# Optimization experiments

Measured on AMD Instinct MI355X. Metric: run time of the kernel, lower is better.

Reference implementation:

```python
import jax, jax.numpy as jnp
import numpy as np

B, N, C = 8, 4096, 768
H = 4 * C  # mlp hidden
EPS = 1e-7
LN_EPS = 1e-5


def _ln(x, g, b):
    mu = jnp.mean(x, axis=-1, keepdims=True)
    var = jnp.mean((x - mu) ** 2, axis=-1, keepdims=True)
    return (x - mu) * jax.lax.rsqrt(var + LN_EPS) * g + b


def _mlp(z, w1, b1, w2, b2):
    return jax.nn.gelu(z @ w1 + b1, approximate=False) @ w2 + b2


def setup_inputs() -> dict:
    key = jax.random.key(0)
    ks = jax.random.split(key, 16)
    s = 1.0 / np.sqrt(C)
    inp = {
        "x": jax.random.normal(ks[0], (B, N, C), jnp.float32),
        "y": jax.random.normal(ks[1], (B, N, C), jnp.float32),
        "mask": jax.random.randint(ks[2], (B, N, 1), 0, 2).astype(jnp.float32),
        "h": 64,
        "w": 64,
        "ln1_g": jnp.ones((C,), jnp.float32),
        "ln1_b": jnp.zeros((C,), jnp.float32),
        "Wq": jax.random.normal(ks[3], (C, C), jnp.float32) * s,
        "Wk": jax.random.normal(ks[4], (C, C), jnp.float32) * s,
        "Wv": jax.random.normal(ks[5], (C, C), jnp.float32) * s,
        "Wpx": jax.random.normal(ks[6], (2 * C, C), jnp.float32) * s,
        "Wpy": jax.random.normal(ks[7], (2 * C, C), jnp.float32) * s,
        "ln2_g": jnp.ones((C,), jnp.float32),
        "ln2_b": jnp.zeros((C,), jnp.float32),
        "fx1_w": jax.random.normal(ks[8], (C, H), jnp.float32) * s,
        "fx1_b": jnp.zeros((H,), jnp.float32),
        "fx2_w": jax.random.normal(ks[9], (H, C), jnp.float32) / np.sqrt(H),
        "fx2_b": jnp.zeros((C,), jnp.float32),
        "fy1_w": jax.random.normal(ks[10], (C, H), jnp.float32) * s,
        "fy1_b": jnp.zeros((H,), jnp.float32),
        "fy2_w": jax.random.normal(ks[11], (H, C), jnp.float32) / np.sqrt(H),
        "fy2_b": jnp.zeros((C,), jnp.float32),
    }
    return inp


def _minmax(s):
    mn = jnp.min(s, axis=1, keepdims=True)
    mx = jnp.max(s, axis=1, keepdims=True)
    return (s - mn) / (mx - mn + EPS)


def reference(x, y, mask, h, w, ln1_g, ln1_b, Wq, Wk, Wv, Wpx, Wpy,
              ln2_g, ln2_b, fx1_w, fx1_b, fx2_w, fx2_b, fy1_w, fy1_b, fy2_w, fy2_b):
    b, n, c = x.shape
    m = mask.reshape(b, n, 1)  # binary mask per token
    xn = _ln(x, ln1_g, ln1_b)
    yn = _ln(y, ln1_g, ln1_b)
    q = yn @ Wq  # (b,n,c)
    k = xn @ Wk
    v = xn @ Wv
    # masked GAP pools (Weighted_GAP): (b,c)
    fg = jnp.sum(q * m, axis=1) / (jnp.sum(m, axis=1) + 5e-4)
    bg = jnp.sum(q * (1.0 - m), axis=1) / (jnp.sum(1.0 - m, axis=1) + 5e-4)
    k_nrm = jnp.linalg.norm(k, axis=2)  # (b,n)
    fg_nrm = jnp.linalg.norm(fg, axis=1, keepdims=True)  # (b,1)
    bg_nrm = jnp.linalg.norm(bg, axis=1, keepdims=True)
    fg_s = jnp.einsum('bnc,bc->bn', k, fg) / (k_nrm * fg_nrm + EPS)
    bg_s = jnp.einsum('bnc,bc->bn', k, bg) / (k_nrm * bg_nrm + EPS)
    scores = _minmax(fg_s) - _minmax(bg_s)  # (b,n)
    pseudo_mask = scores.reshape(b, 1, h, w)
    attn = jax.nn.softmax(jnp.where(scores < 0, scores - 100.0, scores), axis=1)
    query_pro = jnp.einsum('bn,bnc->bc', attn, v)  # (b,c)
    qp_nrm = jnp.linalg.norm(query_pro, axis=1, keepdims=True)
    sim = jnp.sum(query_pro * fg, axis=1, keepdims=True) / (qp_nrm * fg_nrm + EPS)
    sim = (sim + 1.0) * 0.5  # (b,1)
    pro = sim * fg + (1.0 - sim) * query_pro  # (b,c)
    pro_b = jnp.broadcast_to(pro[:, None, :], x.shape)
    xo = x + jnp.concatenate([x, pro_b], axis=-1) @ Wpx
    yo = y + jnp.concatenate([y, pro_b], axis=-1) @ Wpy
    xo = xo + _mlp(_ln(xo, ln2_g, ln2_b), fx1_w, fx1_b, fx2_w, fx2_b)
    yo = yo + _mlp(_ln(yo, ln2_g, ln2_b), fy1_w, fy1_b, fy2_w, fy2_b)
    return (xo, yo, pseudo_mask)
```

## Files before the change

kernel.cpp:

```cpp
#include <hip/hip_runtime.h>
#include <math.h>

#define B_ 8
#define N_ 4096
#define C_ 768
#define H_ 3072
#define M_ (B_*N_)
#define NSPLIT 16

typedef unsigned short u16;
typedef unsigned int u32;
typedef __attribute__((ext_vector_type(8))) __bf16 bf16x8;
typedef __attribute__((ext_vector_type(4))) float f32x4;
typedef __attribute__((ext_vector_type(4))) unsigned short u16x4;
typedef __attribute__((ext_vector_type(8))) unsigned short u16x8;

__device__ __forceinline__ u16 f2bf(float f){
  u32 u = __float_as_uint(f);
  u32 r = (u + 0x7FFFu + ((u >> 16) & 1u)) >> 16;
  return (u16)r;
}
__device__ __forceinline__ float bf2f(u16 h){
  return __uint_as_float(((u32)h) << 16);
}
__device__ __forceinline__ void gload_lds16(const void* g, void* l){
  __builtin_amdgcn_global_load_lds((const __attribute__((address_space(1))) void*)g,
                                   (__attribute__((address_space(3))) void*)l, 16, 0, 0);
}

template<int EPI>
__global__ __launch_bounds__(512, 4) void gemm_bf16(
    const u16* __restrict__ A, const u16* __restrict__ BT,
    int K, int N, int NBN,
    void* __restrict__ outp,
    const float* __restrict__ resid,
    const float* __restrict__ rowv,
    const float* __restrict__ bias)
{
  __shared__ u16 lds[2][12288];
  const int tid = threadIdx.x;
  const int wid = tid >> 6, lane = tid & 63;

  const int nwg = gridDim.x;
  int wg = blockIdx.x;
  wg = (wg & 7) * (nwg >> 3) + (wg >> 3);
  const int GMN = 8 * NBN;
  const int g = wg / GMN, r = wg % GMN;
  const int bm = (g*8 + (r & 7)) * 256;
  const int bn = (r >> 3) * 128;

  const int wr = wid >> 1, wc = wid & 1;

  f32x4 acc[4][4];
#pragma unroll
  for (int i=0;i<4;i++)
#pragma unroll
    for (int j=0;j<4;j++) acc[i][j] = (f32x4){0.f,0.f,0.f,0.f};

  const u16* agp0 = A  + (size_t)(bm + (tid>>2))*K + (tid&3)*8;
  const u16* agp1 = A  + (size_t)(bm + 128 + (tid>>2))*K + (tid&3)*8;
  const u16* bgp0 = BT + (size_t)(bn + (tid>>2))*K + (tid&3)*8;

  auto STAGE = [&](int c){
    char* base = (char*)lds[c] + wid*1024;
    gload_lds16(agp0, base);
    gload_lds16(agp1, base + 8192);
    gload_lds16(bgp0, base + 16384);
    agp0 += 32; agp1 += 32; bgp0 += 32;
  };

  const int aoff = (wr*64 + (lane&15))*32 + ((lane>>4)<<3);
  const int boff = 8192 + (wc*64 + (lane&15))*32 + ((lane>>4)<<3);

  const int nk = K >> 5;
  STAGE(0);
  __syncthreads();
  int cur = 0;
  for (int kk=0; kk<nk; kk++){
    if (kk+1 < nk) STAGE(cur^1);
    bf16x8 av[4], bv[4];
    const u16* pa = &lds[cur][aoff];
    const u16* pb = &lds[cur][boff];
#pragma unroll
    for (int i=0;i<4;i++){
      av[i] = *reinterpret_cast<const bf16x8*>(pa + i*512);
      bv[i] = *reinterpret_cast<const bf16x8*>(pb + i*512);
    }
#pragma unroll
    for (int i=0;i<4;i++)
#pragma unroll
      for (int j=0;j<4;j++)
        acc[i][j] = __builtin_amdgcn_mfma_f32_16x16x32_bf16(av[i], bv[j], acc[i][j], 0, 0, 0);
    __syncthreads();
    cur ^= 1;
  }

  const int col0 = bn + wc*64 + (lane & 15);
  const int row0 = bm + wr*64 + ((lane >> 4) << 2);
#pragma unroll
  for (int i=0;i<4;i++){
#pragma unroll
    for (int j=0;j<4;j++){
#pragma unroll
      for (int r2=0;r2<4;r2++){
        const int row = row0 + i*16 + r2;
        const int cj  = col0 + j*16;
        const size_t o = (size_t)row*N + cj;
        const float va = acc[i][j][r2];
        if constexpr (EPI == 0){
          ((u16*)outp)[o] = f2bf(va);
        } else if constexpr (EPI == 1){
          ((float*)outp)[o] = resid[o] + va + rowv[(row >> 12)*N + cj];
        } else if constexpr (EPI == 2){
          const float z = va + bias[cj];
          ((u16*)outp)[o] = f2bf(0.5f*z*(1.0f + erff(z*0.70710678f)));
        } else {
          float* po = (float*)outp + o;
          *po += va + bias[cj];
        }
      }
    }
  }
}

__device__ __forceinline__ void ln_row(const float* __restrict__ p,
    const float* __restrict__ gam, const float* __restrict__ bet,
    u16* __restrict__ op, int lane)
{
  float4 v0 = *reinterpret_cast<const float4*>(p + lane*4);
  float4 v1 = *reinterpret_cast<const float4*>(p + lane*4 + 256);
  float4 v2 = *reinterpret_cast<const float4*>(p + lane*4 + 512);
  float s  = v0.x+v0.y+v0.z+v0.w + v1.x+v1.y+v1.z+v1.w + v2.x+v2.y+v2.z+v2.w;
  float sq = v0.x*v0.x+v0.y*v0.y+v0.z*v0.z+v0.w*v0.w
           + v1.x*v1.x+v1.y*v1.y+v1.z*v1.z+v1.w*v1.w
           + v2.x*v2.x+v2.y*v2.y+v2.z*v2.z+v2.w*v2.w;
#pragma unroll
  for (int o=32;o>0;o>>=1){ s += __shfl_xor(s,o); sq += __shfl_xor(sq,o); }
  const float mu = s * (1.f/C_);
  const float rs = rsqrtf(sq*(1.f/C_) - mu*mu + 1e-5f);
  float4 g0 = *reinterpret_cast<const float4*>(gam + lane*4);
  float4 g1 = *reinterpret_cast<const float4*>(gam + lane*4 + 256);
  float4 g2 = *reinterpret_cast<const float4*>(gam + lane*4 + 512);
  float4 b0 = *reinterpret_cast<const float4*>(bet + lane*4);
  float4 b1 = *reinterpret_cast<const float4*>(bet + lane*4 + 256);
  float4 b2 = *reinterpret_cast<const float4*>(bet + lane*4 + 512);
  u16x4 o0, o1, o2;
  o0[0]=f2bf((v0.x-mu)*rs*g0.x+b0.x); o0[1]=f2bf((v0.y-mu)*rs*g0.y+b0.y);
  o0[2]=f2bf((v0.z-mu)*rs*g0.z+b0.z); o0[3]=f2bf((v0.w-mu)*rs*g0.w+b0.w);
  o1[0]=f2bf((v1.x-mu)*rs*g1.x+b1.x); o1[1]=f2bf((v1.y-mu)*rs*g1.y+b1.y);
  o1[2]=f2bf((v1.z-mu)*rs*g1.z+b1.z); o1[3]=f2bf((v1.w-mu)*rs*g1.w+b1.w);
  o2[0]=f2bf((v2.x-mu)*rs*g2.x+b2.x); o2[1]=f2bf((v2.y-mu)*rs*g2.y+b2.y);
  o2[2]=f2bf((v2.z-mu)*rs*g2.z+b2.z); o2[3]=f2bf((v2.w-mu)*rs*g2.w+b2.w);
  *reinterpret_cast<u16x4*>(op + lane*4)       = o0;
  *reinterpret_cast<u16x4*>(op + lane*4 + 256) = o1;
  *reinterpret_cast<u16x4*>(op + lane*4 + 512) = o2;
}

__global__ __launch_bounds__(256) void ln_fwd(const float* __restrict__ in,
    const float* __restrict__ gam, const float* __restrict__ bet,
    u16* __restrict__ out)
{
  const int row  = blockIdx.x*4 + (threadIdx.x >> 6);
  const int lane = threadIdx.x & 63;
  ln_row(in + (size_t)row*C_, gam, bet, out + (size_t)row*C_, lane);
}

__global__ __launch_bounds__(256) void ln_fwd2(const float* __restrict__ inx,
    const float* __restrict__ iny, const float* __restrict__ gam,
    const float* __restrict__ bet, u16* __restrict__ outx, u16* __restrict__ outy)
{
  const int row  = blockIdx.x*4 + (threadIdx.x >> 6);
  const int lane = threadIdx.x & 63;
  const float* in = blockIdx.y ? iny : inx;
  u16* out = blockIdx.y ? outy : outx;
  ln_row(in + (size_t)row*C_, gam, bet, out + (size_t)row*C_, lane);
}

__global__ __launch_bounds__(256) void cvt2_bf16(const float* __restrict__ inx,
    const float* __restrict__ iny, u16* __restrict__ outx, u16* __restrict__ outy,
    int n4)
{
  int i = blockIdx.x*256 + threadIdx.x;
  const float* in = blockIdx.y ? iny : inx;
  u16* out = blockIdx.y ? outy : outx;
  if (i < n4){
    float4 v = reinterpret_cast<const float4*>(in)[i];
    u16x4 o; o[0]=f2bf(v.x); o[1]=f2bf(v.y); o[2]=f2bf(v.z); o[3]=f2bf(v.w);
    *reinterpret_cast<u16x4*>(out + (size_t)i*4) = o;
  }
}

__device__ __forceinline__ void tr_tile(const float* __restrict__ in,
    u16* __restrict__ outp, int R, int Cc, int t)
{
  __shared__ float tile[32][33];
  const int tilesx = Cc >> 5;
  const int c0 = (t % tilesx)*32, r0 = (t / tilesx)*32;
  const int tx = threadIdx.x & 31, ty = threadIdx.x >> 5;
#pragma unroll
  for (int i=0;i<32;i+=8)
    tile[ty+i][tx] = in[(size_t)(r0+ty+i)*Cc + c0+tx];
  __syncthreads();
#pragma unroll
  for (int i=0;i<32;i+=8)
    outp[(size_t)(c0+ty+i)*R + r0+tx] = f2bf(tile[tx][ty+i]);
}

__global__ __launch_bounds__(256) void transpose_all(
    const float* Wk, const float* Wpx, const float* Wpy,
    const float* f1x, const float* f2x, const float* f1y, const float* f2y,
    u16* WkT, u16* WpxT, u16* WpyT, u16* f1xT, u16* f2xT, u16* f1yT, u16* f2yT)
{
  int t = blockIdx.x;
  if (t < 1728){
    const int m = t / 576; t -= m*576;
    const float* in = (m==0)?Wk:((m==1)?Wpx:Wpy);
    u16* o = (m==0)?WkT:((m==1)?WpxT:WpyT);
    tr_tile(in, o, C_, C_, t);
  } else {
    t -= 1728;
    const int m = t / 2304; t -= m*2304;
    if (m==0)      tr_tile(f1x, f1xT, C_, H_, t);
    else if (m==1) tr_tile(f2x, f2xT, H_, C_, t);
    else if (m==2) tr_tile(f1y, f1yT, C_, H_, t);
    else           tr_tile(f2y, f2yT, H_, C_, t);
  }
}

__global__ __launch_bounds__(256) void pool_partial(const u16* __restrict__ q,
    const float* __restrict__ mask, float* __restrict__ pm, float* __restrict__ pa,
    float* __restrict__ mpart)
{
  const int c = blockIdx.x*256 + threadIdx.x;
  const int b = blockIdx.y, z = blockIdx.z;
  const int n0 = z*(N_/NSPLIT);
  const u16* qp = q + ((size_t)b*N_ + n0)*C_ + c;
  const float* mp = mask + (size_t)b*N_ + n0;
  float am=0.f, aa=0.f, ms=0.f;
  for (int n=0;n<N_/NSPLIT;n++){
    float v = bf2f(qp[(size_t)n*C_]);
    float m = mp[n];
    am += v*m; aa += v; ms += m;
  }
  const size_t o = ((size_t)z*B_ + b)*C_ + c;
  pm[o]=am; pa[o]=aa;
  if (blockIdx.x==0 && threadIdx.x==0) mpart[z*B_+b] = ms;
}

__global__ __launch_bounds__(256) void proto_fused(const float* __restrict__ pm,
    const float* __restrict__ pa, const float* __restrict__ mpart,
    const float* __restrict__ Wq,
    float* __restrict__ fg, float* __restrict__ bg,
    float* __restrict__ fgn, float* __restrict__ bgn)
{
  __shared__ float fin[C_], bin[C_];
  __shared__ float red[8];
  const int b = blockIdx.x, tid = threadIdx.x;
  float msum_b = 0.f;
#pragma unroll
  for (int z=0;z<NSPLIT;z++) msum_b += mpart[z*B_+b];
  for (int c=tid;c<C_;c+=256){
    float sm=0.f, sa=0.f;
#pragma unroll
    for (int z=0;z<NSPLIT;z++){ size_t o=((size_t)z*B_+b)*C_+c; sm+=pm[o]; sa+=pa[o]; }
    fin[c] = sm/(msum_b + 5e-4f);
    bin[c] = (sa - sm)/((float)N_ - msum_b + 5e-4f);
  }
  __syncthreads();
  const int j0 = tid, j1 = tid+256, j2 = tid+512;
  float f0=0,f1=0,f2=0,g0=0,g1=0,g2=0;
  for (int c=0;c<C_;c++){
    const float* w = Wq + (size_t)c*C_;
    float fc = fin[c], bc = bin[c];
    float w0=w[j0], w1=w[j1], w2=w[j2];
    f0 += fc*w0; f1 += fc*w1; f2 += fc*w2;
    g0 += bc*w0; g1 += bc*w1; g2 += bc*w2;
  }
  fg[b*C_+j0]=f0; fg[b*C_+j1]=f1; fg[b*C_+j2]=f2;
  bg[b*C_+j0]=g0; bg[b*C_+j1]=g1; bg[b*C_+j2]=g2;
  float sf = f0*f0+f1*f1+f2*f2, sb = g0*g0+g1*g1+g2*g2;
#pragma unroll
  for (int o=32;o>0;o>>=1){ sf+=__shfl_down(sf,o); sb+=__shfl_down(sb,o); }
  if ((tid&63)==0){ red[tid>>6]=sf; red[4+(tid>>6)]=sb; }
  __syncthreads();
  if (tid==0){
    fgn[b]=sqrtf(red[0]+red[1]+red[2]+red[3]);
    bgn[b]=sqrtf(red[4]+red[5]+red[6]+red[7]);
  }
}

__global__ __launch_bounds__(256) void score_kernel(const u16* __restrict__ k,
    const float* __restrict__ fg, const float* __restrict__ bg,
    const float* __restrict__ fgn, const float* __restrict__ bgn,
    float* __restrict__ fg_s, float* __restrict__ bg_s)
{
  const int t = blockIdx.x*4 + (threadIdx.x >> 6);
  const int lane = threadIdx.x & 63;
  const int b = t >> 12;
  const u16* kp = k + (size_t)t*C_;
  u16x8 k8 = *reinterpret_cast<const u16x8*>(kp + lane*8);
  u16x4 k4 = *reinterpret_cast<const u16x4*>(kp + 512 + lane*4);
  const float* fgp = fg + b*C_;
  const float* bgp = bg + b*C_;
  float4 fa = *reinterpret_cast<const float4*>(fgp + lane*8);
  float4 fb = *reinterpret_cast<const float4*>(fgp + lane*8 + 4);
  float4 fc = *reinterpret_cast<const float4*>(fgp + 512 + lane*4);
  float4 ba = *reinterpret_cast<const float4*>(bgp + lane*8);
  float4 bb = *reinterpret_cast<const float4*>(bgp + lane*8 + 4);
  float4 bc = *reinterpret_cast<const float4*>(bgp + 512 + lane*4);
  float kv[12];
#pragma unroll
  for (int i=0;i<8;i++) kv[i] = bf2f(k8[i]);
#pragma unroll
  for (int i=0;i<4;i++) kv[8+i] = bf2f(k4[i]);
  float df = kv[0]*fa.x+kv[1]*fa.y+kv[2]*fa.z+kv[3]*fa.w
           + kv[4]*fb.x+kv[5]*fb.y+kv[6]*fb.z+kv[7]*fb.w
           + kv[8]*fc.x+kv[9]*fc.y+kv[10]*fc.z+kv[11]*fc.w;
  float db = kv[0]*ba.x+kv[1]*ba.y+kv[2]*ba.z+kv[3]*ba.w
           + kv[4]*bb.x+kv[5]*bb.y+kv[6]*bb.z+kv[7]*bb.w
           + kv[8]*bc.x+kv[9]*bc.y+kv[10]*bc.z+kv[11]*bc.w;
  float kk=0.f;
#pragma unroll
  for (int i=0;i<12;i++) kk += kv[i]*kv[i];
#pragma unroll
  for (int o=32;o>0;o>>=1){
    df+=__shfl_xor(df,o); db+=__shfl_xor(db,o); kk+=__shfl_xor(kk,o);
  }
  if (lane==0){
    const float kn = sqrtf(kk);
    fg_s[t] = df/(kn*fgn[b]+1e-7f);
    bg_s[t] = db/(kn*bgn[b]+1e-7f);
  }
}

__global__ __launch_bounds__(256) void minmax_kernel(const float* __restrict__ fg_s,
    const float* __restrict__ bg_s, float* __restrict__ mm)
{
  __shared__ float sm[16];
  const int b = blockIdx.x;
  float mnf=1e30f, mxf=-1e30f, mnb=1e30f, mxb=-1e30f;
  for (int i=threadIdx.x;i<N_;i+=256){
    float a = fg_s[(size_t)b*N_+i]; mnf=fminf(mnf,a); mxf=fmaxf(mxf,a);
    float c = bg_s[(size_t)b*N_+i]; mnb=fminf(mnb,c); mxb=fmaxf(mxb,c);
  }
#pragma unroll
  for (int o=32;o>0;o>>=1){
    mnf=fminf(mnf,__shfl_down(mnf,o)); mxf=fmaxf(mxf,__shfl_down(mxf,o));
    mnb=fminf(mnb,__shfl_down(mnb,o)); mxb=fmaxf(mxb,__shfl_down(mxb,o));
  }
  const int wid = threadIdx.x>>6;
  if ((threadIdx.x&63)==0){ sm[wid]=mnf; sm[4+wid]=mxf; sm[8+wid]=mnb; sm[12+wid]=mxb; }
  __syncthreads();
  if (threadIdx.x==0){
    mm[b*4+0]=fminf(fminf(sm[0],sm[1]),fminf(sm[2],sm[3]));
    mm[b*4+1]=fmaxf(fmaxf(sm[4],sm[5]),fmaxf(sm[6],sm[7]));
    mm[b*4+2]=fminf(fminf(sm[8],sm[9]),fminf(sm[10],sm[11]));
    mm[b*4+3]=fmaxf(fmaxf(sm[12],sm[13]),fmaxf(sm[14],sm[15]));
  }
}

__global__ __launch_bounds__(1024) void scorefin_fused(const float* __restrict__ fg_s,
    const float* __restrict__ bg_s, const float* __restrict__ mm,
    float* __restrict__ pseudo, float* __restrict__ escr, float* __restrict__ denom)
{
  __shared__ float sm[16];
  const int b = blockIdx.x, tid = threadIdx.x;
  const float mnf=mm[b*4+0], mxf=mm[b*4+1], mnb=mm[b*4+2], mxb=mm[b*4+3];
  const float rf = 1.f/(mxf-mnf+1e-7f), rb = 1.f/(mxb-mnb+1e-7f);
  float ps = 0.f;
#pragma unroll
  for (int i=0;i<4;i++){
    const int t = tid + i*1024;
    const size_t o = (size_t)b*N_ + t;
    const float s = (fg_s[o]-mnf)*rf - (bg_s[o]-mnb)*rb;
    pseudo[o] = s;
    const float e = expf(s < 0.f ? s - 100.f : s);
    escr[o] = e;
    ps += e;
  }
#pragma unroll
  for (int o=32;o>0;o>>=1) ps += __shfl_down(ps,o);
  if ((tid&63)==0) sm[tid>>6]=ps;
  __syncthreads();
  if (tid==0){
    float s=0.f;
#pragma unroll
    for (int w=0;w<16;w++) s+=sm[w];
    denom[b]=s;
  }
}

__global__ __launch_bounds__(256) void vpool_partial(const u16* __restrict__ xn,
    const float* __restrict__ e, float* __restrict__ pv)
{
  const int c = blockIdx.x*256 + threadIdx.x;
  const int b = blockIdx.y, z = blockIdx.z;
  const int n0 = z*(N_/NSPLIT);
  const u16* vp = xn + ((size_t)b*N_ + n0)*C_ + c;
  const float* ep = e + (size_t)b*N_ + n0;
  float acc=0.f;
  for (int n=0;n<N_/NSPLIT;n++) acc += bf2f(vp[(size_t)n*C_])*ep[n];
  pv[((size_t)z*B_+b)*C_+c] = acc;
}

__global__ __launch_bounds__(256) void pro_fused(const float* __restrict__ pv,
    const float* __restrict__ denom,
    const float* __restrict__ Wv, const float* __restrict__ Wpx,
    const float* __restrict__ Wpy,
    const float* __restrict__ fg, const float* __restrict__ fgn,
    float* __restrict__ rowx, float* __restrict__ rowy)
{
  __shared__ float vin[C_];
  __shared__ float red[8];
  __shared__ float simsh;
  const int b = blockIdx.x, tid = threadIdx.x;
  const float den = 1.f/denom[b];
  for (int c=tid;c<C_;c+=256){
    float s=0.f;
#pragma unroll
    for (int z=0;z<NSPLIT;z++) s += pv[((size_t)z*B_+b)*C_+c];
    vin[c] = s*den;
  }
  __syncthreads();
  const int j0 = tid, j1 = tid+256, j2 = tid+512;
  float q0=0,q1=0,q2=0;
  for (int c=0;c<C_;c++){
    const float* w = Wv + (size_t)c*C_;
    float vv = vin[c];
    q0 += vv*w[j0]; q1 += vv*w[j1]; q2 += vv*w[j2];
  }
  const float fg0 = fg[b*C_+j0], fg1 = fg[b*C_+j1], fg2 = fg[b*C_+j2];
  float d = q0*fg0 + q1*fg1 + q2*fg2;
  float qq = q0*q0 + q1*q1 + q2*q2;
#pragma unroll
  for (int o=32;o>0;o>>=1){ d+=__shfl_down(d,o); qq+=__shfl_down(qq,o); }
  if ((tid&63)==0){ red[tid>>6]=d; red[4+(tid>>6)]=qq; }
  __syncthreads();
  if (tid==0){
    float dd=red[0]+red[1]+red[2]+red[3], qs=red[4]+red[5]+red[6]+red[7];
    simsh = (dd/(sqrtf(qs)*fgn[b]+1e-7f)+1.f)*0.5f;
  }
  __syncthreads();
  const float sim = simsh;
  vin[j0] = sim*fg0 + (1.f-sim)*q0;
  vin[j1] = sim*fg1 + (1.f-sim)*q1;
  vin[j2] = sim*fg2 + (1.f-sim)*q2;
  __syncthreads();
  float rx0=0,rx1=0,rx2=0, ry0=0,ry1=0,ry2=0;
  for (int c=0;c<C_;c++){
    const float* wx = Wpx + (size_t)(C_+c)*C_;
    const float* wy = Wpy + (size_t)(C_+c)*C_;
    float pc = vin[c];
    rx0 += pc*wx[j0]; rx1 += pc*wx[j1]; rx2 += pc*wx[j2];
    ry0 += pc*wy[j0]; ry1 += pc*wy[j1]; ry2 += pc*wy[j2];
  }
  rowx[b*C_+j0]=rx0; rowx[b*C_+j1]=rx1; rowx[b*C_+j2]=rx2;
  rowy[b*C_+j0]=ry0; rowy[b*C_+j1]=ry1; rowy[b*C_+j2]=ry2;
}

extern "C" void kernel_launch(void* const* d_in, const int* in_sizes, int n_in,
                              void* d_out, int out_size, void* d_ws, size_t ws_size,
                              hipStream_t stream)
{
  const float* x     = (const float*)d_in[0];
  const float* y     = (const float*)d_in[1];
  const float* mask  = (const float*)d_in[2];
  const float* ln1_g = (const float*)d_in[5];
  const float* ln1_b = (const float*)d_in[6];
  const float* Wq    = (const float*)d_in[7];
  const float* Wk    = (const float*)d_in[8];
  const float* Wv    = (const float*)d_in[9];
  const float* Wpx   = (const float*)d_in[10];
  const float* Wpy   = (const float*)d_in[11];
  const float* ln2_g = (const float*)d_in[12];
  const float* ln2_b = (const float*)d_in[13];
  const float* fx1_w = (const float*)d_in[14];
  const float* fx1_b = (const float*)d_in[15];
  const float* fx2_w = (const float*)d_in[16];
  const float* fx2_b = (const float*)d_in[17];
  const float* fy1_w = (const float*)d_in[18];
  const float* fy1_b = (const float*)d_in[19];
  const float* fy2_w = (const float*)d_in[20];
  const float* fy2_b = (const float*)d_in[21];

  float* out    = (float*)d_out;
  float* out_xo = out;
  float* out_yo = out + (size_t)M_*C_;
  float* out_ps = out + 2*(size_t)M_*C_;

  char* ws = (char*)d_ws;
  const size_t ACT = (size_t)M_*C_;
  u16* R0  = (u16*)ws;
  u16* xnb = R0;
  u16* ynb = R0 + ACT;
  u16* kb  = R0 + 2*ACT;
  u16* hid = R0;
  u16* qb  = (u16*)(ws + 4*ACT*2);
  u16* wp  = (u16*)(ws + 5*ACT*2);
  u16* WkT  = wp;
  u16* WpxT = wp + 1*589824;
  u16* WpyT = wp + 2*589824;
  u16* fx1T = wp + 3*589824;
  u16* fx2T = fx1T + 2359296;
  u16* fy1T = fx2T + 2359296;
  u16* fy2T = fy1T + 2359296;
  float* st   = (float*)(ws + 5*ACT*2 + (size_t)(3*589824 + 4*2359296)*2);
  float* fgn  = st + 8;
  float* bgn  = st + 16;
  float* denom= st + 24;
  float* mm   = st + 32;
  float* fg   = st + 64;
  float* bg   = st + 6208;
  float* rowx = st + 24640;
  float* rowy = st + 30784;
  float* fg_s = st + 37056;
  float* bg_s = st + 69824;
  float* escr = st + 102592;
  float* pm   = st + 135360;
  float* pa   = st + 233664;
  float* pv   = st + 331968;
  float* mpart= st + 430272;

  dim3 tb(256);
  dim3 tg(512);

  transpose_all<<<dim3(10944),tb,0,stream>>>(Wk,Wpx,Wpy,fx1_w,fx2_w,fy1_w,fy2_w,
                                             WkT,WpxT,WpyT,fx1T,fx2T,fy1T,fy2T);
  ln_fwd2<<<dim3(M_/4,2),tb,0,stream>>>(x, y, ln1_g, ln1_b, xnb, ynb);

  gemm_bf16<0><<<dim3(128*6),tg,0,stream>>>(xnb, WkT, C_, C_, 6, kb, nullptr,nullptr,nullptr);

  pool_partial<<<dim3(3,B_,NSPLIT),tb,0,stream>>>(ynb, mask, pm, pa, mpart);
  proto_fused<<<B_,tb,0,stream>>>(pm, pa, mpart, Wq, fg, bg, fgn, bgn);

  score_kernel<<<M_/4,tb,0,stream>>>(kb, fg, bg, fgn, bgn, fg_s, bg_s);
  minmax_kernel<<<B_,tb,0,stream>>>(fg_s, bg_s, mm);
  scorefin_fused<<<B_,dim3(1024),0,stream>>>(fg_s, bg_s, mm, out_ps, escr, denom);

  vpool_partial<<<dim3(3,B_,NSPLIT),tb,0,stream>>>(xnb, escr, pv);
  pro_fused<<<B_,tb,0,stream>>>(pv, denom, Wv, Wpx, Wpy, fg, fgn, rowx, rowy);

  cvt2_bf16<<<dim3((ACT/4+255)/256,2),tb,0,stream>>>(x, y, xnb, ynb, (int)(ACT/4));

  gemm_bf16<1><<<dim3(128*6),tg,0,stream>>>(xnb, WpxT, C_, C_, 6, out_xo, x, rowx, nullptr);
  gemm_bf16<1><<<dim3(128*6),tg,0,stream>>>(ynb, WpyT, C_, C_, 6, out_yo, y, rowy, nullptr);

  ln_fwd<<<M_/4,tb,0,stream>>>(out_xo, ln2_g, ln2_b, qb);
  gemm_bf16<2><<<dim3(128*24),tg,0,stream>>>(qb, fx1T, C_, H_, 24, hid, nullptr,nullptr, fx1_b);
  gemm_bf16<3><<<dim3(128*6),tg,0,stream>>>(hid, fx2T, H_, C_, 6, out_xo, nullptr,nullptr, fx2_b);

  ln_fwd<<<M_/4,tb,0,stream>>>(out_yo, ln2_g, ln2_b, qb);
  gemm_bf16<2><<<dim3(128*24),tg,0,stream>>>(qb, fy1T, C_, H_, 24, hid, nullptr,nullptr, fy1_b);
  gemm_bf16<3><<<dim3(128*6),tg,0,stream>>>(hid, fy2T, H_, C_, 6, out_yo, nullptr,nullptr, fy2_b);
}
```

Measured before the change: 1.621 ms.

## Triple-buffer GEMM LDS staging with XOR swizzle to avoid bank conflicts

The bf16 GEMM moves from a double-buffered LDS pipeline to a three-stage ring, prefetching two K-tiles ahead. It waits on vmcnt counters plus a single barrier per iteration instead of two __syncthreads. It also XOR-swizzles the 16-byte chunk placement in the global-load-to-LDS path and the matching reads, aiming to cut LDS bank conflicts. LDS per block grows from 48KB to 72KB, which can lower occupancy relative to the launch bound of 4 blocks.

New measurement: 1.528 ms. 1.06x faster.

```diff
diff --git a/kernel.cpp b/kernel.cpp
--- a/kernel.cpp
+++ b/kernel.cpp
@@ -37,7 +37,7 @@
     const float* __restrict__ rowv,
     const float* __restrict__ bias)
 {
-  __shared__ u16 lds[2][12288];
+  __shared__ u16 lds[3][12288];
   const int tid = threadIdx.x;
   const int wid = tid >> 6, lane = tid & 63;
 
@@ -50,6 +50,7 @@
   const int bn = (r >> 3) * 128;
 
   const int wr = wid >> 1, wc = wid & 1;
+  const int l15 = lane & 15;
 
   f32x4 acc[4][4];
 #pragma unroll
@@ -57,30 +58,40 @@
 #pragma unroll
     for (int j=0;j<4;j++) acc[i][j] = (f32x4){0.f,0.f,0.f,0.f};
 
-  const u16* agp0 = A  + (size_t)(bm + (tid>>2))*K + (tid&3)*8;
-  const u16* agp1 = A  + (size_t)(bm + 128 + (tid>>2))*K + (tid&3)*8;
-  const u16* bgp0 = BT + (size_t)(bn + (tid>>2))*K + (tid&3)*8;
-
-  auto STAGE = [&](int c){
-    char* base = (char*)lds[c] + wid*1024;
+  const int srow = tid >> 2;
+  const int lchq = (tid & 3) ^ ((tid >> 3) & 3);
+  const u16* agp0 = A  + (size_t)(bm + srow)*K       + lchq*8;
+  const u16* agp1 = A  + (size_t)(bm + 128 + srow)*K + lchq*8;
+  const u16* bgp0 = BT + (size_t)(bn + srow)*K       + lchq*8;
+
+  auto STAGE = [&](int bi){
+    char* base = (char*)lds[bi] + wid*1024;
     gload_lds16(agp0, base);
     gload_lds16(agp1, base + 8192);
     gload_lds16(bgp0, base + 16384);
     agp0 += 32; agp1 += 32; bgp0 += 32;
   };
 
-  const int aoff = (wr*64 + (lane&15))*32 + ((lane>>4)<<3);
-  const int boff = 8192 + (wc*64 + (lane&15))*32 + ((lane>>4)<<3);
+  const int arow = wr*64 + l15;
+  const int brow = wc*64 + l15;
+  const int aswz = (arow >> 1) & 3;
+  const int bswz = (brow >> 1) & 3;
+  const int aoff = arow*32 + (((lane>>4) ^ aswz) << 3);
+  const int boff = 8192 + brow*32 + (((lane>>4) ^ bswz) << 3);
 
   const int nk = K >> 5;
   STAGE(0);
-  __syncthreads();
-  int cur = 0;
+  STAGE(1);
+  int cb = 0;
   for (int kk=0; kk<nk; kk++){
-    if (kk+1 < nk) STAGE(cur^1);
+    if (kk == nk-1){ asm volatile("s_waitcnt vmcnt(0)" ::: "memory"); }
+    else           { asm volatile("s_waitcnt vmcnt(3)" ::: "memory"); }
+    __builtin_amdgcn_s_barrier();
+    __builtin_amdgcn_sched_barrier(0);
+    if (kk+2 < nk) STAGE(cb==0 ? 2 : cb-1);
     bf16x8 av[4], bv[4];
-    const u16* pa = &lds[cur][aoff];
-    const u16* pb = &lds[cur][boff];
+    const u16* pa = &lds[cb][aoff];
+    const u16* pb = &lds[cb][boff];
 #pragma unroll
     for (int i=0;i<4;i++){
       av[i] = *reinterpret_cast<const bf16x8*>(pa + i*512);
@@ -91,11 +102,10 @@
 #pragma unroll
       for (int j=0;j<4;j++)
         acc[i][j] = __builtin_amdgcn_mfma_f32_16x16x32_bf16(av[i], bv[j], acc[i][j], 0, 0, 0);
-    __syncthreads();
-    cur ^= 1;
-  }
-
-  const int col0 = bn + wc*64 + (lane & 15);
+    cb = (cb==2) ? 0 : cb+1;
+  }
+
+  const int col0 = bn + wc*64 + l15;
   const int row0 = bm + wr*64 + ((lane >> 4) << 2);
 #pragma unroll
   for (int i=0;i<4;i++){
```
